# Kernel optimization log

Measured on AMD Instinct MI355X. Metric: run time of the kernel, lower is better.

The kernel has to match this reference:

```python
import jax, jax.numpy as jnp
import numpy as np

NEG = -1.0e30  # finite stand-in for -inf (exp(NEG-x)==0 exactly in fp32, grad-safe)
PRUNE = 5


def setup_inputs() -> dict:
    key = jax.random.key(0)
    k1, k2, k3, k4 = jax.random.split(key, 4)
    B, T, U, V = 8, 192, 193, 512
    logits = jax.random.normal(k1, (B, T, U, V), dtype=jnp.float32)
    log_probs = jax.nn.log_softmax(logits, axis=-1)  # [B,T,U,V]
    targets = jax.random.randint(k2, (B, U - 1), 1, V, dtype=jnp.int32)
    # lengths must satisfy |t_len-u_len| <= PRUNE for the terminal cell to be in-band
    target_lengths = jax.random.randint(k3, (B,), 150, U, dtype=jnp.int32)
    off = jax.random.randint(k4, (B,), -3, 4, dtype=jnp.int32)
    logit_lengths = jnp.clip(target_lengths + off, 1, T).astype(jnp.int32)
    return {"log_probs": log_probs, "targets": targets,
            "logit_lengths": logit_lengths, "target_lengths": target_lengths}


def _rnnt_loss(log_probs, targets, logit_lengths, target_lengths, prune_range=PRUNE):
    B, T, U, V = log_probs.shape
    Ut = targets.shape[1]  # U - 1
    dt = log_probs.dtype

    blank = log_probs[..., 0]  # [B,T,U] p_blank at (t,u)
    # emit[b,t,j] = log_probs[b,t,j,targets[b,j]]
    emit = jnp.take_along_axis(log_probs[:, :, :Ut, :], targets[:, None, :, None], axis=3)[..., 0]  # [B,T,Ut]
    # emit candidate requires t < T: pad a NEG row at t==T
    emit = jnp.concatenate([emit, jnp.full((B, 1, Ut), NEG, dt)], axis=1)  # [B,T+1,Ut]
    # g[b,t,u] = gain entering cell (t,u) from (t,u-1); g[:,:,0] unused
    g_all = jnp.concatenate([jnp.full((B, T + 1, 1), NEG, dt), emit], axis=2)  # [B,T+1,U]
    # blank_pad[:,t,:] = blank[:,t-1,:] (row t pulls blank from frame t-1); t==0 has no blank move
    blank_pad = jnp.concatenate([jnp.full((B, 1, U), NEG, dt), blank], axis=1)  # [B,T+1,U]

    u_idx = jnp.arange(U)

    def band_mask(t):
        # cells the original actually computes on row t
        return ((u_idx[None, :] >= t - prune_range)
                & (u_idx[None, :] <= t + prune_range)
                & (u_idx[None, :] <= target_lengths[:, None]))

    def combine(x, y):
        # linear recurrence r[u] = logaddexp(r[u-1] + g[u], base[u]) as an associative op
        g1, r1 = x
        g2, r2 = y
        return (g1 + g2, jnp.logaddexp(r1 + g2, r2))

    def row_from_base(base, g, t):
        base = jnp.where(band_mask(t), base, NEG)  # out-of-band cells never feed the row
        _, r = jax.lax.associative_scan(combine, (g, base), axis=1)
        return jnp.where(band_mask(t), r, NEG)

    # row 0: alpha[0,0]=0, within-row emit chain
    init_base = jnp.full((B, U), NEG, dt).at[:, 0].set(0.0)
    row0 = row_from_base(init_base, g_all[:, 0], 0)

    def step(prev, xs):
        blank_row, g_row, t = xs
        row = row_from_base(prev + blank_row, g_row, t)  # blank move from row t-1, then emit chain
        return row, row

    ts = jnp.arange(1, T + 1)
    _, rows = jax.lax.scan(step, row0,
                           (blank_pad[:, 1:].transpose(1, 0, 2),
                            g_all[:, 1:].transpose(1, 0, 2), ts))
    rows = jnp.concatenate([row0[None], rows], axis=0)  # [T+1,B,U]

    final = rows[logit_lengths, jnp.arange(B), target_lengths]  # alpha[t_len, u_len]
    return jnp.mean(-final)  # reduction='mean'


def reference(log_probs, targets, logit_lengths, target_lengths):
    return _rnnt_loss(log_probs, targets, logit_lengths, target_lengths)
```

## Files before the change

kernel.cpp:

```cpp
#include <hip/hip_runtime.h>


#define NEGV -1.0e30f
#define LOG2E 1.4426950408889634f
#define LN2   0.6931471805599453f

constexpr int Bc = 8, Tc = 192, Uc = 193, Vc = 512;
constexpr int Utc = Uc - 1;
constexpr int ROWS = Tc + 1;

#if __has_builtin(__builtin_amdgcn_exp2f)
#define EXP2(x) __builtin_amdgcn_exp2f(x)
#else
#define EXP2(x) __expf((x) * LN2)
#endif
#if __has_builtin(__builtin_amdgcn_logf)
#define LOG2(x) __builtin_amdgcn_logf(x)
#else
#define LOG2(x) (__logf(x) * LOG2E)
#endif

template <int CTRL>
__device__ __forceinline__ float dppf(float old, float x) {
    return __int_as_float(__builtin_amdgcn_update_dpp(
        __float_as_int(old), __float_as_int(x), CTRL, 0xF, 0xF, false));
}

__device__ __forceinline__ float lae2(float a, float b) {
    float m = fmaxf(a, b);
    float d = fminf(a, b) - m;
    return m + LOG2(1.0f + EXP2(d));
}

__device__ __forceinline__ float prefix_sum16(float g) {
    g += dppf<0x111>(0.0f, g);
    g += dppf<0x112>(0.0f, g);
    g += dppf<0x114>(0.0f, g);
    g += dppf<0x118>(0.0f, g);
    return g;
}

__global__ void __launch_bounds__(1024) rnnt_fused_kernel(
        const float* __restrict__ lp, const int* __restrict__ targets,
        const int* __restrict__ logit_len, const int* __restrict__ target_len,
        float* __restrict__ out) {
    __shared__ float2 rowbuf[ROWS * 16];

    const int b = blockIdx.x;
    const int tlen = target_len[b];
    const int llen = logit_len[b];
    const int nrows = llen + 1;

    for (int idx = threadIdx.x; idx < nrows * 16; idx += 1024) {
        int t = idx >> 4, d = idx & 15;
        int u = t - 5 + d;
        float bl = NEGV;
        float g = 0.0f;
        if (d <= 10 && u >= 0 && u <= Uc - 1 && t >= 1)
            bl = lp[(((size_t)b * Tc + (t - 1)) * Uc + u) * Vc] * LOG2E;
        if (d <= 10 && u >= 1 && u <= Uc - 1 && t <= Tc - 1)
            g = lp[(((size_t)b * Tc + t) * Uc + (u - 1)) * Vc + targets[b * Utc + (u - 1)]] * LOG2E;
        rowbuf[idx] = make_float2(bl, g);
    }
    __syncthreads();
    if (threadIdx.x >= 64) return;

    const int lane = threadIdx.x;
    const int ls = lane & 15;

    float alpha = NEGV;
    float2 cur = rowbuf[ls];
    float G = prefix_sum16(cur.y);
    float2 nxt;

    for (int t = 0; t <= llen; ++t) {
        if (t < llen) nxt = rowbuf[(t + 1) * 16 + ls];

        float base;
        if (t == 0) {
            base = (lane == 5) ? 0.0f : NEGV;
        } else {
            float prevA = dppf<0x101>(NEGV, alpha);
            base = prevA + cur.x;
        }

        float r;
        if (t == Tc) {
            r = base;
        } else {
            float s = base - G;
            s = lae2(dppf<0x111>(NEGV, s), s);
            s = lae2(dppf<0x112>(NEGV, s), s);
            s = lae2(dppf<0x114>(NEGV, s), s);
            s = lae2(dppf<0x118>(NEGV, s), s);
            r = s + G;
        }

        int u = t - 5 + lane;
        bool valid = (lane <= 10) && (u >= 0) && (u <= tlen);
        alpha = valid ? r : NEGV;

        if (t < llen) { cur = nxt; G = prefix_sum16(cur.y); }
    }

    if (lane == tlen - llen + 5)
        atomicAdd(out, alpha * (-LN2 / (float)Bc));
}

extern "C" void kernel_launch(void* const* d_in, const int* in_sizes, int n_in,
                              void* d_out, int out_size, void* d_ws, size_t ws_size,
                              hipStream_t stream) {
    const float* lp    = (const float*)d_in[0];
    const int* targets = (const int*)d_in[1];
    const int* llen    = (const int*)d_in[2];
    const int* tlen    = (const int*)d_in[3];
    float* out = (float*)d_out;

    hipMemsetAsync(out, 0, sizeof(float) * out_size, stream);
    rnnt_fused_kernel<<<Bc, 1024, 0, stream>>>(lp, targets, llen, tlen, out);
}
```

Before: 686.0 us.

## Split time recurrence into parallel chunks composed via log-semiring transfer matrices

The sequential scan over T rows per batch is replaced by 16 time-chunks per batch. Each chunk runs the band recurrence from 11 unit basis vectors at once to build an 11x11 log-space transfer matrix, and a second kernel chains the 16 matrices with a vector-matrix log-sum-exp product. This exposes parallelism across many blocks and shortens the serial dependency chain, including the gather latency that each batch previously paid alone. In exchange it does about 11x more recurrence arithmetic, adds a second kernel launch, and passes the matrices through workspace memory.

```diff
diff --git a/kernel.cpp b/kernel.cpp
--- a/kernel.cpp
+++ b/kernel.cpp
@@ -7,7 +7,8 @@
 
 constexpr int Bc = 8, Tc = 192, Uc = 193, Vc = 512;
 constexpr int Utc = Uc - 1;
-constexpr int ROWS = Tc + 1;
+constexpr int NCH = 16;
+constexpr int CL  = 12;
 
 #if __has_builtin(__builtin_amdgcn_exp2f)
 #define EXP2(x) __builtin_amdgcn_exp2f(x)
@@ -40,71 +41,123 @@
     return g;
 }
 
-__global__ void __launch_bounds__(1024) rnnt_fused_kernel(
+__device__ __forceinline__ float prefix_lae16(float s) {
+    s = lae2(dppf<0x111>(NEGV, s), s);
+    s = lae2(dppf<0x112>(NEGV, s), s);
+    s = lae2(dppf<0x114>(NEGV, s), s);
+    s = lae2(dppf<0x118>(NEGV, s), s);
+    return s;
+}
+
+__device__ __forceinline__ float row_update(float alpha, float2 cur, int t,
+                                            int tlen, int ls) {
+    float base = dppf<0x101>(NEGV, alpha) + cur.x;
+    float res;
+    if (t == Tc) {
+        res = base;
+    } else {
+        float G = prefix_sum16(cur.y);
+        res = prefix_lae16(base - G) + G;
+    }
+    int u = t - 5 + ls;
+    bool valid = (ls <= 10) && (u >= 0) && (u <= tlen);
+    return valid ? res : NEGV;
+}
+
+__global__ void __launch_bounds__(192) rnnt_chunk_kernel(
         const float* __restrict__ lp, const int* __restrict__ targets,
         const int* __restrict__ logit_len, const int* __restrict__ target_len,
-        float* __restrict__ out) {
-    __shared__ float2 rowbuf[ROWS * 16];
+        float* __restrict__ ws) {
+    __shared__ float2 rowbuf[CL * 16];
 
-    const int b = blockIdx.x;
+    const int b = blockIdx.x >> 4;
+    const int c = blockIdx.x & 15;
+    const int llen = logit_len[b];
     const int tlen = target_len[b];
-    const int llen = logit_len[b];
-    const int nrows = llen + 1;
+    const int t0 = 1 + c * CL;
 
-    for (int idx = threadIdx.x; idx < nrows * 16; idx += 1024) {
-        int t = idx >> 4, d = idx & 15;
-        int u = t - 5 + d;
-        float bl = NEGV;
-        float g = 0.0f;
-        if (d <= 10 && u >= 0 && u <= Uc - 1 && t >= 1)
-            bl = lp[(((size_t)b * Tc + (t - 1)) * Uc + u) * Vc] * LOG2E;
-        if (d <= 10 && u >= 1 && u <= Uc - 1 && t <= Tc - 1)
-            g = lp[(((size_t)b * Tc + t) * Uc + (u - 1)) * Vc + targets[b * Utc + (u - 1)]] * LOG2E;
-        rowbuf[idx] = make_float2(bl, g);
+    {
+        const int idx = threadIdx.x;
+        const int r = idx >> 4, d = idx & 15;
+        const int t = t0 + r;
+        if (t <= llen) {
+            const int u = t - 5 + d;
+            float bl = NEGV;
+            float g = 0.0f;
+            if (d <= 10 && u >= 0 && u <= Uc - 1)
+                bl = lp[(((size_t)b * Tc + (t - 1)) * Uc + u) * Vc] * LOG2E;
+            if (d <= 10 && u >= 1 && u <= Uc - 1 && t <= Tc - 1)
+                g = lp[(((size_t)b * Tc + t) * Uc + (u - 1)) * Vc
+                       + targets[b * Utc + (u - 1)]] * LOG2E;
+            rowbuf[idx] = make_float2(bl, g);
+        }
     }
     __syncthreads();
-    if (threadIdx.x >= 64) return;
 
+    const int j  = threadIdx.x >> 4;
+    const int ls = threadIdx.x & 15;
+    if (j >= 11) return;
+
+    float alpha = (ls == j) ? 0.0f : NEGV;
+    #pragma unroll
+    for (int r = 0; r < CL; ++r) {
+        const int t = t0 + r;
+        if (t > llen) break;
+        alpha = row_update(alpha, rowbuf[r * 16 + ls], t, tlen, ls);
+    }
+    ws[(((size_t)(b * NCH + c) * 11 + j) << 4) + ls] = alpha;
+}
+
+__global__ void __launch_bounds__(64) rnnt_final_kernel(
+        const float* __restrict__ lp, const int* __restrict__ targets,
+        const int* __restrict__ logit_len, const int* __restrict__ target_len,
+        const float* __restrict__ ws, float* __restrict__ out) {
+    const int b = blockIdx.x;
+    const int llen = logit_len[b];
+    const int tlen = target_len[b];
     const int lane = threadIdx.x;
     const int ls = lane & 15;
 
-    float alpha = NEGV;
-    float2 cur = rowbuf[ls];
-    float G = prefix_sum16(cur.y);
-    float2 nxt;
+    float g = 0.0f;
+    {
+        const int u = ls - 5;
+        if (ls <= 10 && u >= 1)
+            g = lp[((size_t)b * Tc * Uc + (u - 1)) * Vc
+                   + targets[b * Utc + (u - 1)]] * LOG2E;
+    }
+    float v;
+    {
+        float G = prefix_sum16(g);
+        float base = (ls == 5) ? 0.0f : NEGV;
+        float res = prefix_lae16(base - G) + G;
+        const int u = ls - 5;
+        const bool valid = (ls <= 10) && (u >= 0) && (u <= tlen);
+        v = valid ? res : NEGV;
+    }
 
-    for (int t = 0; t <= llen; ++t) {
-        if (t < llen) nxt = rowbuf[(t + 1) * 16 + ls];
-
-        float base;
-        if (t == 0) {
-            base = (lane == 5) ? 0.0f : NEGV;
-        } else {
-            float prevA = dppf<0x101>(NEGV, alpha);
-            base = prevA + cur.x;
+    for (int c = 0; c < NCH; ++c) {
+        const size_t off = ((size_t)(b * NCH + c) * 11) << 4;
+        float cand[11];
+        #pragma unroll
+        for (int jj = 0; jj < 11; ++jj) {
+            float m = ws[off + ((size_t)jj << 4) + ls];
+            float vj = __int_as_float(
+                __builtin_amdgcn_readlane(__float_as_int(v), jj));
+            cand[jj] = m + vj;
         }
-
-        float r;
-        if (t == Tc) {
-            r = base;
-        } else {
-            float s = base - G;
-            s = lae2(dppf<0x111>(NEGV, s), s);
-            s = lae2(dppf<0x112>(NEGV, s), s);
-            s = lae2(dppf<0x114>(NEGV, s), s);
-            s = lae2(dppf<0x118>(NEGV, s), s);
-            r = s + G;
-        }
-
-        int u = t - 5 + lane;
-        bool valid = (lane <= 10) && (u >= 0) && (u <= tlen);
-        alpha = valid ? r : NEGV;
-
-        if (t < llen) { cur = nxt; G = prefix_sum16(cur.y); }
+        float a0 = lae2(cand[0], cand[1]);
+        float a1 = lae2(cand[2], cand[3]);
+        float a2 = lae2(cand[4], cand[5]);
+        float a3 = lae2(cand[6], cand[7]);
+        float a4 = lae2(cand[8], cand[9]);
+        float b0 = lae2(a0, a1);
+        float b1 = lae2(a2, a3);
+        float b2 = lae2(a4, cand[10]);
+        v = lae2(lae2(b0, b1), b2);
     }
 
     if (lane == tlen - llen + 5)
-        atomicAdd(out, alpha * (-LN2 / (float)Bc));
+        atomicAdd(out, v * (-LN2 / (float)Bc));
 }
 
 extern "C" void kernel_launch(void* const* d_in, const int* in_sizes, int n_in,
@@ -117,5 +170,8 @@
     float* out = (float*)d_out;
 
     hipMemsetAsync(out, 0, sizeof(float) * out_size, stream);
-    rnnt_fused_kernel<<<Bc, 1024, 0, stream>>>(lp, targets, llen, tlen, out);
+    rnnt_chunk_kernel<<<Bc * NCH, 192, 0, stream>>>(
+        lp, targets, llen, tlen, (float*)d_ws);
+    rnnt_final_kernel<<<Bc, 64, 0, stream>>>(
+        lp, targets, llen, tlen, (const float*)d_ws, out);
 }
```

After: 648.5 us. 1.06x faster.
